# Optimization experiments

Measured on AMD Instinct MI355X. Metric: run time of the kernel, lower is better.

Reference implementation:

```python
import jax, jax.numpy as jnp
import numpy as np
from itertools import combinations

ADD = 4          # max subset size (init kwarg `add`)
N_FEAT = 12      # number of input columns
BATCH = 32768


def setup_inputs() -> dict:
    key = jax.random.key(0)
    x = jax.random.uniform(key, (BATCH, N_FEAT), dtype=jnp.float32)  # values in [0,1]
    lambda_ = jnp.float32(0.3)  # learnable Schweizer-Sklar exponent
    return {"x": x, "lambda_": lambda_}


def reference(x, lambda_):
    # x: [B, n] in [0,1]. For every column subset of size 2..ADD (lexicographic,
    # matching itertools.combinations), fold the Schweizer-Sklar t-norm:
    #   h <- 1 - ((1-h)^L + (1-s)^L - (1-h)^L * (1-s)^L)^(1/L)
    # Vectorized across all combinations of a given size; the fold over the
    # (<= ADD-1) elements of each subset stays a tiny static Python loop.
    n = x.shape[1]
    inv = 1.0 / lambda_
    outs = [x]
    for size in range(2, ADD + 1):
        idx = np.array(list(combinations(range(n), size)), dtype=np.int32)  # [K, size]
        sub = x[:, idx]            # [B, K, size]
        hidden = sub[..., 0]       # [B, K]
        for j in range(1, size):
            a = (1.0 - hidden) ** lambda_
            b = (1.0 - sub[..., j]) ** lambda_
            hidden = 1.0 - (a + b - a * b) ** inv
        outs.append(hidden)
    # [B, n + C(n,2) + ... + C(n,ADD)] = [B, 793]
    return jnp.concatenate(outs, axis=1)
```

## Files before the change

kernel.cpp:

```cpp
#include <hip/hip_runtime.h>

#define NFEAT 12
#define NCOMB 781
#define NCOLS 793
#define BLOCK 256

struct Tab { unsigned short v[NCOMB]; };

constexpr Tab make_tab() {
    Tab t{};
    int k = 0;
    for (int a = 0; a < 12; a++)
        for (int b = a + 1; b < 12; b++)
            t.v[k++] = (unsigned short)(a | (b << 4) | (12 << 8) | (12 << 12));
    for (int a = 0; a < 12; a++)
        for (int b = a + 1; b < 12; b++)
            for (int c = b + 1; c < 12; c++)
                t.v[k++] = (unsigned short)(a | (b << 4) | (c << 8) | (12 << 12));
    for (int a = 0; a < 12; a++)
        for (int b = a + 1; b < 12; b++)
            for (int c = b + 1; c < 12; c++)
                for (int d = c + 1; d < 12; d++)
                    t.v[k++] = (unsigned short)(a | (b << 4) | (c << 8) | (d << 12));
    return t;
}

__constant__ Tab c_tab = make_tab();

__device__ __forceinline__ float fast_pow1m(float one_minus_base, float e) {
    return __builtin_exp2f(e * __builtin_log2f(one_minus_base));
}

__global__ __launch_bounds__(BLOCK) void schweizer_kernel(
        const float* __restrict__ x,
        const float* __restrict__ lam_p,
        float* __restrict__ out) {
    const int row = blockIdx.x;
    const int tid = threadIdx.x;

    __shared__ float sp[16];
    __shared__ float sx[NFEAT];

    const float lam = lam_p[0];
    const float inv = 1.0f / lam;

    if (tid < 16) sp[tid] = 1.0f;
    __syncthreads();
    if (tid < NFEAT) {
        float xv = x[row * NFEAT + tid];
        sx[tid] = xv;
        sp[tid] = 1.0f - fast_pow1m(1.0f - xv, lam);
    }
    __syncthreads();

    float* orow = out + (size_t)row * NCOLS;

    #pragma unroll
    for (int base = 0; base < NCOLS; base += BLOCK) {
        int col = base + tid;
        if (col >= NCOLS) break;
        float v;
        if (col < NFEAT) {
            v = sx[col];
        } else {
            unsigned e = c_tab.v[col - NFEAT];
            float prod = sp[e & 15] * sp[(e >> 4) & 15]
                       * sp[(e >> 8) & 15] * sp[(e >> 12) & 15];
            v = 1.0f - fast_pow1m(1.0f - prod, inv);
        }
        orow[col] = v;
    }
}

extern "C" void kernel_launch(void* const* d_in, const int* in_sizes, int n_in,
                              void* d_out, int out_size, void* d_ws, size_t ws_size,
                              hipStream_t stream) {
    const float* x   = (const float*)d_in[0];
    const float* lam = (const float*)d_in[1];
    float* out       = (float*)d_out;
    const int batch  = in_sizes[0] / NFEAT;
    schweizer_kernel<<<batch, BLOCK, 0, stream>>>(x, lam, out);
}
```

Before: 140.2 us.

## Process eight rows per block with vectorized nontemporal float4 stores

```diff
diff --git a/kernel.cpp b/kernel.cpp
--- a/kernel.cpp
+++ b/kernel.cpp
@@ -3,7 +3,12 @@
 #define NFEAT 12
 #define NCOMB 781
 #define NCOLS 793
+#define ROWS_PB 8
 #define BLOCK 256
+#define CHUNK_ELEMS (ROWS_PB * NCOLS)
+#define CHUNK_VEC4  (CHUNK_ELEMS / 4)
+
+typedef float f32x4 __attribute__((ext_vector_type(4)));
 
 struct Tab { unsigned short v[NCOMB]; };
 
@@ -27,48 +32,57 @@
 
 __constant__ Tab c_tab = make_tab();
 
-__device__ __forceinline__ float fast_pow1m(float one_minus_base, float e) {
-    return __builtin_exp2f(e * __builtin_log2f(one_minus_base));
+__device__ __forceinline__ float fast_pow(float b, float e) {
+    return __builtin_exp2f(e * __builtin_log2f(b));
 }
 
 __global__ __launch_bounds__(BLOCK) void schweizer_kernel(
         const float* __restrict__ x,
         const float* __restrict__ lam_p,
         float* __restrict__ out) {
-    const int row = blockIdx.x;
-    const int tid = threadIdx.x;
+    const int chunk = blockIdx.x;
+    const int tid   = threadIdx.x;
 
-    __shared__ float sp[16];
-    __shared__ float sx[NFEAT];
+    __shared__ float sp[ROWS_PB * 16];
+    __shared__ float sx[ROWS_PB * NFEAT];
 
     const float lam = lam_p[0];
     const float inv = 1.0f / lam;
 
-    if (tid < 16) sp[tid] = 1.0f;
+    if (tid < ROWS_PB * 16) sp[tid] = 1.0f;
     __syncthreads();
-    if (tid < NFEAT) {
-        float xv = x[row * NFEAT + tid];
+    if (tid < ROWS_PB * NFEAT) {
+        float xv = x[(size_t)chunk * ROWS_PB * NFEAT + tid];
+        int r = tid / NFEAT;
+        int c = tid - r * NFEAT;
         sx[tid] = xv;
-        sp[tid] = 1.0f - fast_pow1m(1.0f - xv, lam);
+        sp[r * 16 + c] = 1.0f - fast_pow(1.0f - xv, lam);
     }
     __syncthreads();
 
-    float* orow = out + (size_t)row * NCOLS;
+    f32x4* ovec = (f32x4*)(out + (size_t)chunk * CHUNK_ELEMS);
 
-    #pragma unroll
-    for (int base = 0; base < NCOLS; base += BLOCK) {
-        int col = base + tid;
-        if (col >= NCOLS) break;
-        float v;
-        if (col < NFEAT) {
-            v = sx[col];
-        } else {
-            unsigned e = c_tab.v[col - NFEAT];
-            float prod = sp[e & 15] * sp[(e >> 4) & 15]
-                       * sp[(e >> 8) & 15] * sp[(e >> 12) & 15];
-            v = 1.0f - fast_pow1m(1.0f - prod, inv);
+    for (int v4 = tid; v4 < CHUNK_VEC4; v4 += BLOCK) {
+        int f = v4 * 4;
+        int r = f / NCOLS;
+        int c = f - r * NCOLS;
+        f32x4 o;
+        #pragma unroll
+        for (int j = 0; j < 4; j++) {
+            float val;
+            if (c < NFEAT) {
+                val = sx[r * NFEAT + c];
+            } else {
+                unsigned e = c_tab.v[c - NFEAT];
+                const float* spr = sp + r * 16;
+                float prod = spr[e & 15] * spr[(e >> 4) & 15]
+                           * spr[(e >> 8) & 15] * spr[(e >> 12) & 15];
+                val = 1.0f - fast_pow(1.0f - prod, inv);
+            }
+            o[j] = val;
+            if (++c == NCOLS) { c = 0; ++r; }
         }
-        orow[col] = v;
+        __builtin_nontemporal_store(o, ovec + v4);
     }
 }
 
@@ -79,5 +93,6 @@
     const float* lam = (const float*)d_in[1];
     float* out       = (float*)d_out;
     const int batch  = in_sizes[0] / NFEAT;
-    schweizer_kernel<<<batch, BLOCK, 0, stream>>>(x, lam, out);
+    const int nchunk = batch / ROWS_PB;
+    schweizer_kernel<<<nchunk, BLOCK, 0, stream>>>(x, lam, out);
 }
```

Measured after the change: 129.8 us. -7.4%, faster.
